# Optimization experiments

Hardware: AMD Instinct MI355X
Metric: run time of the kernel (lower is better)

Reference implementation:

```python
import jax, jax.numpy as jnp
import numpy as np

L = 6        # num_coupling_layers
T_DIM = 64   # t_dim
HALF = T_DIM // 2
COND = 128   # cond_dim
HID = 1024   # hidden_dim
B = 32768


def setup_inputs() -> dict:
    key = jax.random.key(0)
    ks = jax.random.split(key, 8)
    s_in = 1.0 / np.sqrt(HALF + COND)
    s_h = 1.0 / np.sqrt(HID)
    T = jax.random.normal(ks[0], (B, T_DIM), dtype=jnp.float32)
    cond = jax.random.normal(ks[1], (B, COND), dtype=jnp.float32)
    W1 = jax.random.normal(ks[2], (L, HALF + COND, HID), dtype=jnp.float32) * s_in
    b1 = jnp.zeros((L, HID), dtype=jnp.float32)
    W2 = jax.random.normal(ks[3], (L, HID, HID), dtype=jnp.float32) * s_h
    b2 = jnp.zeros((L, HID), dtype=jnp.float32)
    W3 = jax.random.normal(ks[4], (L, HID, 2 * HALF), dtype=jnp.float32) * s_h
    b3 = jnp.zeros((L, 2 * HALF), dtype=jnp.float32)
    return {"T": T, "cond": cond, "W1": W1, "b1": b1, "W2": W2, "b2": b2, "W3": W3, "b3": b3}


def reference(T, cond, W1, b1, W2, b2, W3, b3):
    # Conditional normalizing flow: 6 affine coupling layers with alternating
    # contiguous half masks. Even layers transform the first half, odd the second.
    def mlp(h, i):
        x = jax.nn.relu(h @ W1[i] + b1[i])
        x = jax.nn.relu(x @ W2[i] + b2[i])
        return x @ W3[i] + b3[i]

    z = T
    log_det = jnp.zeros(T.shape[0], dtype=T.dtype)
    for i in range(L):
        if i % 2 == 0:
            masked, unmasked = z[:, :HALF], z[:, HALF:]
        else:
            masked, unmasked = z[:, HALF:], z[:, :HALF]
        params = mlp(jnp.concatenate([unmasked, cond], axis=1), i)
        s = jnp.tanh(params[:, :HALF])
        t_shift = params[:, HALF:]
        y_masked = masked * jnp.exp(s) + t_shift
        if i % 2 == 0:
            z = jnp.concatenate([y_masked, unmasked], axis=1)
        else:
            z = jnp.concatenate([unmasked, y_masked], axis=1)
        log_det = log_det + jnp.sum(s, axis=1)
    return z, log_det
```

## Files before the change

### kernel.cpp

```cpp
#include <hip/hip_runtime.h>
#include <hip/hip_fp16.h>
#include <stdint.h>

typedef _Float16 f16;
typedef _Float16 f16x8 __attribute__((ext_vector_type(8)));
typedef float f32x4 __attribute__((ext_vector_type(4)));

#define NB 32768
#define LAYERS 6
#define AK 160
#define HID 1024

__device__ __forceinline__ void async_copy16(const void* g, void* l) {
  __builtin_amdgcn_global_load_lds(
      (const __attribute__((address_space(1))) void*)g,
      (__attribute__((address_space(3))) void*)l, 16, 0, 0);
}

__device__ __forceinline__ void wtrans_tile(const float* __restrict__ W,
                                            f16* __restrict__ Wt,
                                            const int K_, const int N_,
                                            const int bx, const int by,
                                            const int bz, float (*t)[65])
{
  const long off = (long)bz * K_ * N_;
  const float* Wl = W + off;
  f16* Wtl = Wt + off;
  const int k0 = by * 64, n0 = bx * 64;
  const int tx = threadIdx.x & 63, ty4 = threadIdx.x >> 6;
#pragma unroll
  for (int r = ty4; r < 64; r += 4) {
    const int k = k0 + r;
    if (k < K_) t[r][tx] = Wl[(long)k * N_ + n0 + tx];
  }
  __syncthreads();
  const int k = k0 + tx;
  if (k < K_) {
#pragma unroll
    for (int r = ty4; r < 64; r += 4) {
      const int n = n0 + r;
      Wtl[(long)n * K_ + k] = (f16)t[tx][r];
    }
  }
}

__global__ void prep_all(const float* __restrict__ T, const float* __restrict__ cond,
                         const float* __restrict__ W1, const float* __restrict__ W2,
                         const float* __restrict__ W3,
                         float* __restrict__ z, float* __restrict__ ld,
                         f16* __restrict__ A,
                         f16* __restrict__ W1t, f16* __restrict__ W2t,
                         f16* __restrict__ W3t)
{
  __shared__ float t[64][65];
  const int b = blockIdx.x;
  if (b < 2048) {
    const int S1 = NB * 64;
    const int S2 = S1 + NB;
    const int S3 = S2 + NB * 32;
    const int S4 = S3 + NB * 128;
    for (int i = b * blockDim.x + threadIdx.x; i < S4; i += 2048 * blockDim.x) {
      if (i < S1) {
        z[i] = T[i];
      } else if (i < S2) {
        ld[i - S1] = 0.0f;
      } else if (i < S3) {
        int r = i - S2;
        int row = r >> 5, j = r & 31;
        A[(size_t)row * AK + j] = (f16)T[row * 64 + 32 + j];
      } else {
        int r = i - S3;
        int row = r >> 7, j = r & 127;
        A[(size_t)row * AK + 32 + j] = (f16)cond[r];
      }
    }
  } else if (b < 2048 + 288) {
    const int l = b - 2048;
    wtrans_tile(W1, W1t, AK, 1024, l % 16, (l / 16) % 3, l / 48, t);
  } else if (b < 2048 + 288 + 1536) {
    const int l = b - (2048 + 288);
    wtrans_tile(W2, W2t, HID, 1024, l % 16, (l / 16) % 16, l / 256, t);
  } else {
    const int l = b - (2048 + 288 + 1536);
    wtrans_tile(W3, W3t, HID, 64, 0, l % 16, l / 16, t);
  }
}

__global__ __launch_bounds__(256, 2)
void gemm1_full(const f16* __restrict__ A,
                const f16* __restrict__ Wt,
                const float* __restrict__ bias,
                f16* __restrict__ C)
{
  __shared__ __align__(16) f16 As[128 * 160];
  __shared__ __align__(16) f16 Bs[128 * 160];
  const int tid  = threadIdx.x;
  const int lane = tid & 63;
  const int wave = tid >> 6;
  const int c15  = lane & 15;
  const int quad = lane >> 4;
  const int wm = (wave & 1) * 64;
  const int wn = (wave >> 1) * 64;

  const int b = blockIdx.x;
  const int x = b & 7, i = b >> 3;
  const long rowStart = (long)(x * 32 + (i >> 3)) * 128;
  const long colStart = (long)(i & 7) * 128;

  const f16* Ab = A  + rowStart * AK;
  const f16* Bb = Wt + colStart * AK;

#pragma unroll
  for (int it = 0; it < 10; ++it) {
    const int f = it * 256 + tid;
    const int row = f / 20;
    const int ch  = f - row * 20;
    const int chs = ch ^ ((row >> 1) & 3);
    async_copy16(Ab + (long)row * AK + chs * 8, &As[0] + (long)f * 8);
    async_copy16(Bb + (long)row * AK + chs * 8, &Bs[0] + (long)f * 8);
  }
  __syncthreads();

  f32x4 acc[4][4] = {};
#pragma unroll
  for (int kt = 0; kt < 5; ++kt) {
    f16x8 a[4], bf[4];
#pragma unroll
    for (int mi = 0; mi < 4; ++mi) {
      const int R = wm + mi * 16 + c15;
      a[mi] = *(const f16x8*)&As[(R * 20 + kt * 4 + (quad ^ ((R >> 1) & 3))) * 8];
    }
#pragma unroll
    for (int ni = 0; ni < 4; ++ni) {
      const int R = wn + ni * 16 + c15;
      bf[ni] = *(const f16x8*)&Bs[(R * 20 + kt * 4 + (quad ^ ((R >> 1) & 3))) * 8];
    }
#pragma unroll
    for (int mi = 0; mi < 4; ++mi)
#pragma unroll
      for (int ni = 0; ni < 4; ++ni)
        acc[mi][ni] = __builtin_amdgcn_mfma_f32_16x16x32_f16(
            a[mi], bf[ni], acc[mi][ni], 0, 0, 0);
  }

#pragma unroll
  for (int ni = 0; ni < 4; ++ni) {
    const long gn = colStart + wn + ni * 16 + c15;
    const float bv = bias[gn];
#pragma unroll
    for (int mi = 0; mi < 4; ++mi) {
#pragma unroll
      for (int r = 0; r < 4; ++r) {
        const long gm = rowStart + wm + mi * 16 + quad * 4 + r;
        float v = acc[mi][ni][r] + bv;
        v = fmaxf(v, 0.0f);
        C[gm * HID + gn] = (f16)v;
      }
    }
  }
}

__global__ __launch_bounds__(512, 2)
void gemm2_ep(const f16* __restrict__ A,
              const f16* __restrict__ Wt,
              const float* __restrict__ bias,
              f16* __restrict__ C)
{
  __shared__ __align__(16) f16 As[2][16384];
  __shared__ __align__(16) f16 Bs[2][16384];

  const int tid  = threadIdx.x;
  const int lane = tid & 63;
  const int wave = tid >> 6;
  const int c15  = lane & 15;
  const int quad = lane >> 4;
  const int wm = (wave >> 2) * 128;
  const int wn = (wave & 3) * 64;

  const int b = blockIdx.x;
  const int wgid = (b & 7) * 64 + (b >> 3);
  const long rowStart = (long)(wgid >> 2) * 256;
  const long colStart = (long)(wgid & 3) * 256;

  const f16* Ab = A  + rowStart * HID;
  const f16* Bb = Wt + colStart * HID;

  const int rh0 = tid >> 3;
  const int ch0 = tid & 7;
  const long g0 = (long)rh0 * HID + ((ch0 ^ (rh0 & 7)) << 3);
  const long g1 = (long)(64 + rh0) * HID + ((ch0 ^ ((64 + rh0) & 7)) << 3);
  const int l0 = tid << 3;
  const int l1 = (512 + tid) << 3;

  auto stageA = [&](int kt2, int h, int sel) {
    const f16* src = Ab + (long)h * 128 * HID + (long)kt2 * 64;
    f16* dst = &As[sel][h * 8192];
    async_copy16(src + g0, dst + l0);
    async_copy16(src + g1, dst + l1);
  };
  auto stageB = [&](int kt2, int h, int sel) {
    const f16* src = Bb + (long)h * 128 * HID + (long)kt2 * 64;
    f16* dst = &Bs[sel][h * 8192];
    async_copy16(src + g0, dst + l0);
    async_copy16(src + g1, dst + l1);
  };

  stageA(0, 0, 0); stageA(0, 1, 0);
  stageB(0, 0, 0); stageB(0, 1, 0);
  stageB(1, 0, 1); stageA(1, 0, 1);
  asm volatile("s_waitcnt vmcnt(4)" ::: "memory");
  __builtin_amdgcn_s_barrier();
  __builtin_amdgcn_sched_barrier(0);

  f32x4 acc[8][4] = {};

#pragma unroll 2
  for (int kt = 0; kt < 16; ++kt) {
    const int sel = kt & 1;
    const f16* as = &As[sel][0];
    const f16* bs = &Bs[sel][0];
    const bool s1 = (kt + 1 < 16);
    const bool s2 = (kt + 2 < 16);
    f16x8 a0[4][2], a1[4][2], b0[2][2], b1[2][2];

#pragma unroll
    for (int mi = 0; mi < 4; ++mi) {
      const int r = wm + mi * 16 + c15;
#pragma unroll
      for (int ks = 0; ks < 2; ++ks)
        a0[mi][ks] = *(const f16x8*)&as[r * 64 + ((((ks << 2) + quad) ^ (r & 7)) << 3)];
    }
#pragma unroll
    for (int ni = 0; ni < 2; ++ni) {
      const int r = wn + ni * 16 + c15;
#pragma unroll
      for (int ks = 0; ks < 2; ++ks)
        b0[ni][ks] = *(const f16x8*)&bs[r * 64 + ((((ks << 2) + quad) ^ (r & 7)) << 3)];
    }
    if (s1) stageA(kt + 1, 1, sel ^ 1);
    __builtin_amdgcn_s_barrier();
    asm volatile("s_waitcnt lgkmcnt(0)" ::: "memory");
    __builtin_amdgcn_sched_barrier(0);
    __builtin_amdgcn_s_setprio(1);
#pragma unroll
    for (int mi = 0; mi < 4; ++mi)
#pragma unroll
      for (int ni = 0; ni < 2; ++ni)
#pragma unroll
        for (int ks = 0; ks < 2; ++ks)
          acc[mi][ni] = __builtin_amdgcn_mfma_f32_16x16x32_f16(
              a0[mi][ks], b0[ni][ks], acc[mi][ni], 0, 0, 0);
    __builtin_amdgcn_s_setprio(0);
    __builtin_amdgcn_sched_barrier(0);
    __builtin_amdgcn_s_barrier();

#pragma unroll
    for (int ni = 0; ni < 2; ++ni) {
      const int r = wn + 32 + ni * 16 + c15;
#pragma unroll
      for (int ks = 0; ks < 2; ++ks)
        b1[ni][ks] = *(const f16x8*)&bs[r * 64 + ((((ks << 2) + quad) ^ (r & 7)) << 3)];
    }
    if (s1) stageB(kt + 1, 1, sel ^ 1);
    __builtin_amdgcn_s_barrier();
    asm volatile("s_waitcnt lgkmcnt(0)" ::: "memory");
    __builtin_amdgcn_sched_barrier(0);
    __builtin_amdgcn_s_setprio(1);
#pragma unroll
    for (int mi = 0; mi < 4; ++mi)
#pragma unroll
      for (int ni = 0; ni < 2; ++ni)
#pragma unroll
        for (int ks = 0; ks < 2; ++ks)
          acc[mi][2 + ni] = __builtin_amdgcn_mfma_f32_16x16x32_f16(
              a0[mi][ks], b1[ni][ks], acc[mi][2 + ni], 0, 0, 0);
    __builtin_amdgcn_s_setprio(0);
    __builtin_amdgcn_sched_barrier(0);
    __builtin_amdgcn_s_barrier();

#pragma unroll
    for (int mi = 0; mi < 4; ++mi) {
      const int r = wm + 64 + mi * 16 + c15;
#pragma unroll
      for (int ks = 0; ks < 2; ++ks)
        a1[mi][ks] = *(const f16x8*)&as[r * 64 + ((((ks << 2) + quad) ^ (r & 7)) << 3)];
    }
    if (s2) stageB(kt + 2, 0, sel);
    __builtin_amdgcn_s_barrier();
    asm volatile("s_waitcnt lgkmcnt(0)" ::: "memory");
    __builtin_amdgcn_sched_barrier(0);
    __builtin_amdgcn_s_setprio(1);
#pragma unroll
    for (int mi = 0; mi < 4; ++mi)
#pragma unroll
      for (int ni = 0; ni < 2; ++ni)
#pragma unroll
        for (int ks = 0; ks < 2; ++ks)
          acc[4 + mi][ni] = __builtin_amdgcn_mfma_f32_16x16x32_f16(
              a1[mi][ks], b0[ni][ks], acc[4 + mi][ni], 0, 0, 0);
    __builtin_amdgcn_s_setprio(0);
    __builtin_amdgcn_sched_barrier(0);
    __builtin_amdgcn_s_barrier();

    if (s2) stageA(kt + 2, 0, sel);
    __builtin_amdgcn_s_setprio(1);
#pragma unroll
    for (int mi = 0; mi < 4; ++mi)
#pragma unroll
      for (int ni = 0; ni < 2; ++ni)
#pragma unroll
        for (int ks = 0; ks < 2; ++ks)
          acc[4 + mi][2 + ni] = __builtin_amdgcn_mfma_f32_16x16x32_f16(
              a1[mi][ks], b1[ni][ks], acc[4 + mi][2 + ni], 0, 0, 0);
    __builtin_amdgcn_s_setprio(0);
    if (s2) {
      asm volatile("s_waitcnt vmcnt(4)" ::: "memory");
    } else if (s1) {
      asm volatile("s_waitcnt vmcnt(0)" ::: "memory");
    }
    __builtin_amdgcn_sched_barrier(0);
    __builtin_amdgcn_s_barrier();
  }

  f16* Lp = &As[0][0] + wave * 1024;
  const int erow = lane >> 3;
  const int ec   = lane & 7;
  const int ecol8 = ec * 8;
  const long gcol = colStart + wn;
  const int q0x = ((erow >> 2) & 3) << 1;
  const int q1x = (((8 + erow) >> 2) & 3) << 1;
#pragma unroll
  for (int mii = 0; mii < 8; ++mii) {
    const int mof = (mii >> 2) * 64 + (mii & 3) * 16;
#pragma unroll
    for (int nii = 0; nii < 4; ++nii) {
      const int nof = (nii >> 1) * 32 + (nii & 1) * 16;
      const float bv = bias[gcol + nof + c15];
      const int lc = nof + c15;
#pragma unroll
      for (int r = 0; r < 4; ++r) {
        float v = acc[mii][nii][r] + bv;
        Lp[(quad * 4 + r) * 64 + (((lc >> 3) ^ (quad << 1)) << 3) + (lc & 7)]
            = (f16)fmaxf(v, 0.0f);
      }
    }
    f16x8 row0 = *(const f16x8*)&Lp[erow * 64 + ((ec ^ q0x) << 3)];
    f16x8 row1 = *(const f16x8*)&Lp[(8 + erow) * 64 + ((ec ^ q1x) << 3)];
    const long gm0 = rowStart + wm + mof + erow;
    *(f16x8*)&C[gm0 * HID + gcol + ecol8] = row0;
    *(f16x8*)&C[(gm0 + 8) * HID + gcol + ecol8] = row1;
  }
}

__global__ __launch_bounds__(256, 2)
void gemm3_coupling(const f16* __restrict__ X2, const f16* __restrict__ W3t,
                    const float* __restrict__ b3, float* __restrict__ z,
                    float* __restrict__ log_det, f16* __restrict__ Anext,
                    const int maskoff)
{
  __shared__ __align__(16) f16 As[2][64 * 64];
  __shared__ __align__(16) f16 Bs[2][64 * 64];
  const int tid = threadIdx.x;
  const int wave = tid >> 6, lane = tid & 63;
  const int c15 = lane & 15, quad = lane >> 4;
  const int wm = wave * 16;
  const long rowStart = (long)blockIdx.x * 64;

  const f16* Ab = X2 + rowStart * HID;
  const int brow = tid >> 3;
  const int bkc  = ((tid & 7) ^ (brow & 7)) * 8;

  f32x4 acc[4] = {};

  auto stage = [&](int c, int sel) {
    const long kb = (long)c * 64;
#pragma unroll
    for (int q = 0; q < 2; ++q) {
      async_copy16(Ab  + (long)(q * 32 + brow) * HID + kb + bkc,
                   &As[sel][0] + (q * 256 + wave * 64) * 8);
      async_copy16(W3t + (long)(q * 32 + brow) * HID + kb + bkc,
                   &Bs[sel][0] + (q * 256 + wave * 64) * 8);
    }
  };

  stage(0, 0);
  stage(1, 1);
  asm volatile("s_waitcnt vmcnt(4)" ::: "memory");
  __builtin_amdgcn_s_barrier();

  for (int c = 0; c < 16; ++c) {
    const int sel = c & 1;
    const f16* as = &As[sel][0];
    const f16* bs = &Bs[sel][0];

    f16x8 av[2], bv[2][4];
#pragma unroll
    for (int s = 0; s < 2; ++s) {
      const int Ra = wm + c15;
      av[s] = *(const f16x8*)&as[(Ra * 8 + ((s * 4 + quad) ^ (Ra & 7))) * 8];
#pragma unroll
      for (int ni = 0; ni < 4; ++ni) {
        const int R = ni * 16 + c15;
        bv[s][ni] = *(const f16x8*)&bs[(R * 8 + ((s * 4 + quad) ^ (R & 7))) * 8];
      }
    }
    asm volatile("s_waitcnt lgkmcnt(0)" ::: "memory");
    __builtin_amdgcn_s_barrier();
    if (c + 2 < 16) stage(c + 2, sel);

#pragma unroll
    for (int s = 0; s < 2; ++s)
#pragma unroll
      for (int ni = 0; ni < 4; ++ni)
        acc[ni] = __builtin_amdgcn_mfma_f32_16x16x32_f16(av[s], bv[s][ni],
                                                         acc[ni], 0, 0, 0);
    if (c + 2 < 16) {
      asm volatile("s_waitcnt vmcnt(4)" ::: "memory");
    } else if (c + 1 < 16) {
      asm volatile("s_waitcnt vmcnt(0)" ::: "memory");
    }
    __builtin_amdgcn_s_barrier();
  }

  float sp[4] = {0.0f, 0.0f, 0.0f, 0.0f};
#pragma unroll
  for (int ni = 0; ni < 2; ++ni) {
    const int j = ni * 16 + c15;
    const float bs = b3[j];
    const float bt = b3[32 + j];
#pragma unroll
    for (int r = 0; r < 4; ++r) {
      const long gm = rowStart + wm + quad * 4 + r;
      const float sv = acc[ni][r] + bs;
      const float e2 = __expf(2.0f * sv);
      const float s  = 1.0f - 2.0f / (e2 + 1.0f);
      const float tv = acc[ni + 2][r] + bt;
      const float m  = z[gm * 64 + maskoff + j];
      const float y  = fmaf(m, __expf(s), tv);
      z[gm * 64 + maskoff + j] = y;
      Anext[gm * AK + j] = (f16)y;
      sp[r] += s;
    }
  }
#pragma unroll
  for (int r = 0; r < 4; ++r) {
    float v = sp[r];
    v += __shfl_xor(v, 1);
    v += __shfl_xor(v, 2);
    v += __shfl_xor(v, 4);
    v += __shfl_xor(v, 8);
    if (c15 == 0) {
      const long gm = rowStart + wm + quad * 4 + r;
      log_det[gm] += v;
    }
  }
}

extern "C" void kernel_launch(void* const* d_in, const int* in_sizes, int n_in,
                              void* d_out, int out_size, void* d_ws, size_t ws_size,
                              hipStream_t stream) {
  (void)in_sizes; (void)n_in; (void)out_size; (void)ws_size;
  const float* T    = (const float*)d_in[0];
  const float* cond = (const float*)d_in[1];
  const float* W1   = (const float*)d_in[2];
  const float* b1   = (const float*)d_in[3];
  const float* W2   = (const float*)d_in[4];
  const float* b2   = (const float*)d_in[5];
  const float* W3   = (const float*)d_in[6];
  const float* b3   = (const float*)d_in[7];

  float* z  = (float*)d_out;
  float* ld = z + (size_t)NB * 64;

  f16* A   = (f16*)d_ws;
  f16* X1  = A   + (size_t)NB * AK;
  f16* X2  = X1  + (size_t)NB * HID;
  f16* W1t = X2  + (size_t)NB * HID;
  f16* W2t = W1t + (size_t)6 * 1024 * 160;
  f16* W3t = W2t + ((size_t)6 << 20);

  prep_all<<<3968, 256, 0, stream>>>(T, cond, W1, W2, W3,
                                     z, ld, A, W1t, W2t, W3t);

  const int g1 = (NB / 128) * (HID / 128);
  const int g2 = (NB / 256) * (HID / 256);
  for (int l = 0; l < LAYERS; ++l) {
    gemm1_full<<<g1, 256, 0, stream>>>(A, W1t + (size_t)l * 1024 * AK,
                                       b1 + l * 1024, X1);
    gemm2_ep<<<g2, 512, 0, stream>>>(X1, W2t + ((size_t)l << 20),
                                     b2 + l * 1024, X2);
    const int maskoff = (l & 1) ? 32 : 0;
    gemm3_coupling<<<NB / 64, 256, 0, stream>>>(X2, W3t + (size_t)l * 64 * 1024,
                                                b3 + l * 64, z, ld, A, maskoff);
  }
}
```

Measured before the change: 728.5 us.

## Double-buffer gemm1 K-chunks in LDS to overlap loads with MFMA

Replaces the single full-K LDS load in the first GEMM with a two-stage double buffer over 32-wide K chunks, prefetching chunk c+2 while computing chunk c. Shared memory per block drops from 80KB to 32KB, so launch bounds are raised to allow 3 blocks per CU. This is meant to hide global-load latency behind MFMA work and raise occupancy, at the cost of extra barriers and waitcnt synchronisation per chunk.

```diff
diff --git a/kernel.cpp b/kernel.cpp
--- a/kernel.cpp
+++ b/kernel.cpp
@@ -86,14 +86,14 @@
   }
 }
 
-__global__ __launch_bounds__(256, 2)
-void gemm1_full(const f16* __restrict__ A,
-                const f16* __restrict__ Wt,
-                const float* __restrict__ bias,
-                f16* __restrict__ C)
+__global__ __launch_bounds__(256, 3)
+void gemm1_db(const f16* __restrict__ A,
+              const f16* __restrict__ Wt,
+              const float* __restrict__ bias,
+              f16* __restrict__ C)
 {
-  __shared__ __align__(16) f16 As[128 * 160];
-  __shared__ __align__(16) f16 Bs[128 * 160];
+  __shared__ __align__(16) f16 As[2][128 * 32];
+  __shared__ __align__(16) f16 Bs[2][128 * 32];
   const int tid  = threadIdx.x;
   const int lane = tid & 63;
   const int wave = tid >> 6;
@@ -110,37 +110,59 @@
   const f16* Ab = A  + rowStart * AK;
   const f16* Bb = Wt + colStart * AK;
 
-#pragma unroll
-  for (int it = 0; it < 10; ++it) {
-    const int f = it * 256 + tid;
-    const int row = f / 20;
-    const int ch  = f - row * 20;
-    const int chs = ch ^ ((row >> 1) & 3);
-    async_copy16(Ab + (long)row * AK + chs * 8, &As[0] + (long)f * 8);
-    async_copy16(Bb + (long)row * AK + chs * 8, &Bs[0] + (long)f * 8);
-  }
-  __syncthreads();
+  const int r0  = tid >> 2;
+  const int ch0 = tid & 3;
+  const long gA0 = (long)r0 * AK + ((ch0 ^ ((r0 >> 1) & 3)) << 3);
+  const long gA1 = gA0 + (long)64 * AK;
+  const int l0 = tid << 3;
+  const int l1 = (256 + tid) << 3;
+
+  auto stage = [&](int c, int sel) {
+    const long kb = (long)c * 32;
+    async_copy16(Ab + kb + gA0, &As[sel][0] + l0);
+    async_copy16(Ab + kb + gA1, &As[sel][0] + l1);
+    async_copy16(Bb + kb + gA0, &Bs[sel][0] + l0);
+    async_copy16(Bb + kb + gA1, &Bs[sel][0] + l1);
+  };
+
+  stage(0, 0);
+  stage(1, 1);
+  asm volatile("s_waitcnt vmcnt(4)" ::: "memory");
+  __builtin_amdgcn_s_barrier();
 
   f32x4 acc[4][4] = {};
-#pragma unroll
-  for (int kt = 0; kt < 5; ++kt) {
+  for (int c = 0; c < 5; ++c) {
+    const int sel = c & 1;
+    const f16* as = &As[sel][0];
+    const f16* bs = &Bs[sel][0];
+
     f16x8 a[4], bf[4];
 #pragma unroll
     for (int mi = 0; mi < 4; ++mi) {
       const int R = wm + mi * 16 + c15;
-      a[mi] = *(const f16x8*)&As[(R * 20 + kt * 4 + (quad ^ ((R >> 1) & 3))) * 8];
+      a[mi] = *(const f16x8*)&as[R * 32 + ((quad ^ ((R >> 1) & 3)) << 3)];
     }
 #pragma unroll
     for (int ni = 0; ni < 4; ++ni) {
       const int R = wn + ni * 16 + c15;
-      bf[ni] = *(const f16x8*)&Bs[(R * 20 + kt * 4 + (quad ^ ((R >> 1) & 3))) * 8];
-    }
+      bf[ni] = *(const f16x8*)&bs[R * 32 + ((quad ^ ((R >> 1) & 3)) << 3)];
+    }
+    asm volatile("s_waitcnt lgkmcnt(0)" ::: "memory");
+    __builtin_amdgcn_s_barrier();
+    if (c + 2 < 5) stage(c + 2, sel);
+
 #pragma unroll
     for (int mi = 0; mi < 4; ++mi)
 #pragma unroll
       for (int ni = 0; ni < 4; ++ni)
         acc[mi][ni] = __builtin_amdgcn_mfma_f32_16x16x32_f16(
             a[mi], bf[ni], acc[mi][ni], 0, 0, 0);
+    if (c + 2 < 5) {
+      asm volatile("s_waitcnt vmcnt(4)" ::: "memory");
+    } else if (c + 1 < 5) {
+      asm volatile("s_waitcnt vmcnt(0)" ::: "memory");
+    }
+    __builtin_amdgcn_s_barrier();
   }
 
 #pragma unroll
@@ -485,8 +507,8 @@
   const int g1 = (NB / 128) * (HID / 128);
   const int g2 = (NB / 256) * (HID / 256);
   for (int l = 0; l < LAYERS; ++l) {
-    gemm1_full<<<g1, 256, 0, stream>>>(A, W1t + (size_t)l * 1024 * AK,
-                                       b1 + l * 1024, X1);
+    gemm1_db<<<g1, 256, 0, stream>>>(A, W1t + (size_t)l * 1024 * AK,
+                                     b1 + l * 1024, X1);
     gemm2_ep<<<g2, 512, 0, stream>>>(X1, W2t + ((size_t)l << 20),
                                      b2 + l * 1024, X2);
     const int maskoff = (l & 1) ? 32 : 0;
```

After: 731.5 us. About the same (+0.4%).
